# Performance work log

Measured on AMD Instinct MI355X. Metric: run time of the kernel, lower is better.

Reference implementation:

```python
import jax, jax.numpy as jnp
import numpy as np

L, B, E, H = 512, 4, 512, 8
D = E // H  # head_dim = 64


def setup_inputs() -> dict:
    key = jax.random.key(0)
    ks = jax.random.split(key, 7)
    query = jax.random.normal(ks[0], (L, B, E), dtype=jnp.float32)
    relation_k = jax.random.normal(ks[1], (B, L, L, D), dtype=jnp.float32)
    relation_v = jax.random.normal(ks[2], (B, L, L, D), dtype=jnp.float32)
    # xavier-uniform-ish scale for the fused QKV projection
    lim = float(np.sqrt(6.0 / (3 * E + E)))
    in_proj_weight = jax.random.uniform(ks[3], (3 * E, E), jnp.float32, -lim, lim)
    in_proj_bias = jnp.zeros((3 * E,), jnp.float32)
    lim_o = float(np.sqrt(1.0 / E))
    out_proj_weight = jax.random.uniform(ks[4], (E, E), jnp.float32, -lim_o, lim_o)
    out_proj_bias = jnp.zeros((E,), jnp.float32)
    return {
        "query": query,
        "relation_k": relation_k,
        "relation_v": relation_v,
        "in_proj_weight": in_proj_weight,
        "in_proj_bias": in_proj_bias,
        "out_proj_weight": out_proj_weight,
        "out_proj_bias": out_proj_bias,
    }


def reference(query, relation_k, relation_v, in_proj_weight, in_proj_bias,
              out_proj_weight, out_proj_bias):
    # query == key == value (qkv_same path), shape (L, B, E)
    scaling = float(D) ** -0.5
    qkv = query @ in_proj_weight.T + in_proj_bias          # (L, B, 3E)
    q, k, v = jnp.split(qkv, 3, axis=-1)                   # each (L, B, E)
    q = q * scaling

    def to_bhld(t):  # (L, B, E) -> (B, H, L, D)
        return t.reshape(L, B, H, D).transpose(1, 2, 0, 3)

    q, k, v = to_bhld(q), to_bhld(k), to_bhld(v)

    # content scores
    scores = jnp.einsum('bhid,bhjd->bhij', q, k)           # (B, H, L, L)

    # relation_k term: torch does a flat .view of (B*H, L, L, D) -> (B*H*L, D, L)
    # which is a row-major REINTERPRETATION (not a transpose). Replicate via reshape:
    rk = relation_k.reshape(B, L, D, L)                    # per-(b,i) block (L*D,) -> (D, L)
    scores = scores + jnp.einsum('bhid,bidj->bhij', q, rk)

    w = jax.nn.softmax(scores, axis=-1)
    w = jnp.where(jnp.isnan(w), jnp.zeros_like(w), w)      # NaN guard as in original

    out = jnp.einsum('bhij,bhjd->bhid', w, v)              # (B, H, L, D)
    # relation_v term: (B*H*L, 1, L) @ (B*H*L, L, D) -> per-query weighted relation values
    out = out + jnp.einsum('bhij,bijd->bhid', w, relation_v)

    out = out.transpose(2, 0, 1, 3).reshape(L, B, E)       # (B,H,L,D) -> (L,B,E)
    return out @ out_proj_weight.T + out_proj_bias
```

## Files before the change

### kernel.cpp

```cpp
#include <hip/hip_runtime.h>
#include <hip/hip_fp16.h>
#include <stdint.h>


typedef short short8 __attribute__((ext_vector_type(8)));
typedef float f32x4 __attribute__((ext_vector_type(4)));
typedef float f32x2 __attribute__((ext_vector_type(2)));
typedef unsigned short u16x4 __attribute__((ext_vector_type(4)));

static __device__ __forceinline__ uint16_t f2bf(float f) {
  uint32_t u = __float_as_uint(f);
  uint32_t r = (u + 0x7FFFu + ((u >> 16) & 1u)) >> 16;
  return (uint16_t)r;
}
static __device__ __forceinline__ float bf2f(uint16_t h) {
  return __uint_as_float(((uint32_t)h) << 16);
}
static __device__ __forceinline__ short8 ld8(const uint16_t* p) {
  return *(const short8*)p;
}
#define MFMA(a, b, c) __builtin_amdgcn_mfma_f32_16x16x32_bf16((a), (b), (c), 0, 0, 0)

__global__ __launch_bounds__(256) void k_conv_all(
    const float* __restrict__ in_w, const float* __restrict__ query,
    const float* __restrict__ out_w, uint16_t* __restrict__ w_hi,
    uint16_t* __restrict__ w_lo, uint16_t* __restrict__ a_hi,
    uint16_t* __restrict__ a_lo, uint16_t* __restrict__ wo_bf) {
  int e = (blockIdx.x * 256 + threadIdx.x) * 4;
  if (e < 786432) {
    f32x4 v = *(const f32x4*)(in_w + e);
    u16x4 hi, lo;
#pragma unroll
    for (int k = 0; k < 4; ++k) {
      hi[k] = f2bf(v[k]);
      lo[k] = f2bf(v[k] - bf2f(hi[k]));
    }
    *(u16x4*)(w_hi + e) = hi;
    *(u16x4*)(w_lo + e) = lo;
  } else if (e < 786432 + 1048576) {
    int o = e - 786432;
    f32x4 v = *(const f32x4*)(query + o);
    u16x4 hi, lo;
#pragma unroll
    for (int k = 0; k < 4; ++k) {
      hi[k] = f2bf(v[k]);
      lo[k] = f2bf(v[k] - bf2f(hi[k]));
    }
    *(u16x4*)(a_hi + o) = hi;
    *(u16x4*)(a_lo + o) = lo;
  } else {
    int o = e - 1835008;
    f32x4 v = *(const f32x4*)(out_w + o);
    u16x4 hi;
#pragma unroll
    for (int k = 0; k < 4; ++k) hi[k] = f2bf(v[k]);
    *(u16x4*)(wo_bf + o) = hi;
  }
}

__global__ __launch_bounds__(256) void k_inproj(
    const uint16_t* __restrict__ a_hi, const uint16_t* __restrict__ a_lo,
    const uint16_t* __restrict__ w_hi, const uint16_t* __restrict__ w_lo,
    const float* __restrict__ bias, float* __restrict__ q_s,
    uint16_t* __restrict__ q_bf, uint16_t* __restrict__ k_bf,
    uint16_t* __restrict__ v_bf) {
  const int wave = threadIdx.x >> 6, lane = threadIdx.x & 63;
  const int wr = wave >> 1, wc = wave & 1;
  const int rif = lane & 15, kg = lane >> 4;
  const int rbase = blockIdx.x * 64 + wr * 32;
  const int cbase = blockIdx.y * 64 + wc * 32;
  f32x4 acc[2][2] = {};
  for (int ks = 0; ks < 512; ks += 32) {
    int kofs = ks + kg * 8;
    short8 aH[2], aL[2], bH[2], bL[2];
#pragma unroll
    for (int m = 0; m < 2; ++m) {
      size_t idx = (size_t)(rbase + m * 16 + rif) * 512 + kofs;
      aH[m] = ld8(a_hi + idx);
      aL[m] = ld8(a_lo + idx);
    }
#pragma unroll
    for (int n = 0; n < 2; ++n) {
      size_t idx = (size_t)(cbase + n * 16 + rif) * 512 + kofs;
      bH[n] = ld8(w_hi + idx);
      bL[n] = ld8(w_lo + idx);
    }
#pragma unroll
    for (int m = 0; m < 2; ++m)
#pragma unroll
      for (int n = 0; n < 2; ++n) {
        acc[m][n] = MFMA(aH[m], bH[n], acc[m][n]);
        acc[m][n] = MFMA(aH[m], bL[n], acc[m][n]);
        acc[m][n] = MFMA(aL[m], bH[n], acc[m][n]);
      }
  }
#pragma unroll
  for (int m = 0; m < 2; ++m)
#pragma unroll
    for (int n = 0; n < 2; ++n)
#pragma unroll
      for (int r = 0; r < 4; ++r) {
        int row = rbase + m * 16 + kg * 4 + r;
        int col = cbase + n * 16 + rif;
        float val = acc[m][n][r] + bias[col];
        int l = row >> 2, b = row & 3;
        int sel = col >> 9, h = (col >> 6) & 7, d = col & 63;
        size_t oidx = ((size_t)(b * 8 + h) * 512 + l) * 64 + d;
        if (sel == 0) {
          val *= 0.125f;
          q_s[oidx] = val;
          q_bf[oidx] = f2bf(val);
        } else if (sel == 1) {
          k_bf[oidx] = f2bf(val);
        } else {
          v_bf[oidx] = f2bf(val);
        }
      }
}

__global__ __launch_bounds__(256) void k_scores(const uint16_t* __restrict__ q_bf,
                                                const uint16_t* __restrict__ k_bf,
                                                __half* __restrict__ scores) {
  const int bh = blockIdx.x;
  const uint16_t* qb = q_bf + (size_t)bh * 512 * 64;
  const uint16_t* kb = k_bf + (size_t)bh * 512 * 64;
  const int wave = threadIdx.x >> 6, lane = threadIdx.x & 63;
  const int wr = wave >> 1, wc = wave & 1;
  const int rif = lane & 15, kg = lane >> 4;
  const int ibase = blockIdx.y * 64 + wr * 32;
  const int jbase = blockIdx.z * 64 + wc * 32;
  f32x4 acc[2][2] = {};
#pragma unroll
  for (int ks = 0; ks < 64; ks += 32) {
    int kofs = ks + kg * 8;
    short8 A[2], Bb[2];
#pragma unroll
    for (int m = 0; m < 2; ++m) A[m] = ld8(qb + (size_t)(ibase + m * 16 + rif) * 64 + kofs);
#pragma unroll
    for (int n = 0; n < 2; ++n) Bb[n] = ld8(kb + (size_t)(jbase + n * 16 + rif) * 64 + kofs);
#pragma unroll
    for (int m = 0; m < 2; ++m)
#pragma unroll
      for (int n = 0; n < 2; ++n) acc[m][n] = MFMA(A[m], Bb[n], acc[m][n]);
  }
  __half* sc = scores + (size_t)bh * 512 * 512;
#pragma unroll
  for (int m = 0; m < 2; ++m)
#pragma unroll
    for (int n = 0; n < 2; ++n)
#pragma unroll
      for (int r = 0; r < 4; ++r)
        sc[(size_t)(ibase + m * 16 + kg * 4 + r) * 512 + (jbase + n * 16 + rif)] =
            __float2half(acc[m][n][r]);
}

__global__ __launch_bounds__(256, 8) void k_mega(
    const float* __restrict__ relation_k, const float* __restrict__ relation_v,
    const float* __restrict__ q_s, const __half* __restrict__ scores,
    uint16_t* __restrict__ wprob, uint16_t* __restrict__ rv_bf) {
  __shared__ float regA[4096];
  __shared__ float qv[512];
  const int b = blockIdx.x >> 9, i = blockIdx.x & 511;
  const int t = threadIdx.x;
  const int wave = t >> 6, lane = t & 63;
  for (int e = t; e < 512; e += 256) {
    int h = e >> 6, d = e & 63;
    qv[d * 8 + h] = q_s[(((size_t)b * 8 + h) * 512 + i) * 64 + d];
  }
  __syncthreads();
  {
    const float* rkp = relation_k + ((size_t)b * 512 + i) * 32768 + 2 * t;
    f32x2 acc[8] = {};
    for (int d0 = 0; d0 < 64; d0 += 8) {
      f32x2 kv[8];
#pragma unroll
      for (int u = 0; u < 8; ++u) kv[u] = *(const f32x2*)(rkp + (size_t)(d0 + u) * 512);
#pragma unroll
      for (int u = 0; u < 8; ++u) {
        f32x4 qA = *(const f32x4*)&qv[(d0 + u) * 8];
        f32x4 qB = *(const f32x4*)&qv[(d0 + u) * 8 + 4];
#pragma unroll
        for (int h = 0; h < 4; ++h) {
          acc[h].x += qA[h] * kv[u].x;
          acc[h].y += qA[h] * kv[u].y;
          acc[4 + h].x += qB[h] * kv[u].x;
          acc[4 + h].y += qB[h] * kv[u].y;
        }
      }
    }
#pragma unroll
    for (int h = 0; h < 8; ++h) *(f32x2*)&regA[h * 512 + 2 * t] = acc[h];
  }
  __syncthreads();
  float ex[2][8], rsum[2];
#pragma unroll
  for (int hh = 0; hh < 2; ++hh) {
    int h = wave * 2 + hh;
    const __half* srow = scores + (((size_t)b * 8 + h) * 512 + i) * 512;
    float s[8], m = -1e30f;
#pragma unroll
    for (int jj = 0; jj < 8; ++jj) {
      int j = jj * 64 + lane;
      s[jj] = __half2float(srow[j]) + regA[h * 512 + j];
      m = fmaxf(m, s[jj]);
    }
    for (int o = 32; o > 0; o >>= 1) m = fmaxf(m, __shfl_xor(m, o));
    float sum = 0.f;
#pragma unroll
    for (int jj = 0; jj < 8; ++jj) {
      ex[hh][jj] = __expf(s[jj] - m);
      sum += ex[hh][jj];
    }
    for (int o = 32; o > 0; o >>= 1) sum += __shfl_xor(sum, o);
    rsum[hh] = 1.f / sum;
  }
  __syncthreads();
  {
    float* pbf = regA;
#pragma unroll
    for (int jj = 0; jj < 8; ++jj) {
      int j = jj * 64 + lane;
      f32x2 p;
      p.x = ex[0][jj] * rsum[0];
      p.y = ex[1][jj] * rsum[1];
      *(f32x2*)&pbf[j * 8 + wave * 2] = p;
    }
#pragma unroll
    for (int hh = 0; hh < 2; ++hh) {
      int h = wave * 2 + hh;
      uint16_t* wrow = wprob + (((size_t)b * 8 + h) * 512 + i) * 512;
#pragma unroll
      for (int jj = 0; jj < 8; ++jj) wrow[jj * 64 + lane] = f2bf(ex[hh][jj] * rsum[hh]);
    }
  }
  __syncthreads();
  float racc[8] = {};
  {
    const float* pbf = regA;
    const float* rvb = relation_v + ((size_t)b * 512 + i) * 32768;
    const int jb = wave * 128;
    for (int jj = 0; jj < 128; jj += 8) {
      float r[8];
#pragma unroll
      for (int u = 0; u < 8; ++u) r[u] = rvb[(size_t)(jb + jj + u) * 64 + lane];
#pragma unroll
      for (int u = 0; u < 8; ++u) {
        f32x4 w0 = *(const f32x4*)&pbf[(jb + jj + u) * 8];
        f32x4 w1 = *(const f32x4*)&pbf[(jb + jj + u) * 8 + 4];
#pragma unroll
        for (int h = 0; h < 4; ++h) {
          racc[h] += w0[h] * r[u];
          racc[4 + h] += w1[h] * r[u];
        }
      }
    }
  }
  __syncthreads();
#pragma unroll
  for (int h = 0; h < 8; ++h) regA[(wave * 8 + h) * 64 + lane] = racc[h];
  __syncthreads();
  for (int e = t; e < 512; e += 256) {
    int h = e >> 6, d = e & 63;
    float s = regA[(0 * 8 + h) * 64 + d] + regA[(1 * 8 + h) * 64 + d] +
              regA[(2 * 8 + h) * 64 + d] + regA[(3 * 8 + h) * 64 + d];
    rv_bf[((size_t)i * 4 + b) * 512 + h * 64 + d] = f2bf(s);
  }
}

__global__ __launch_bounds__(256) void k_pv(const uint16_t* __restrict__ w_bf,
                                            const uint16_t* __restrict__ v_bf,
                                            uint16_t* __restrict__ pv_bf) {
  const int bh = blockIdx.x;
  const int b = bh >> 3, h = bh & 7;
  const uint16_t* wb = w_bf + (size_t)bh * 512 * 512;
  const uint16_t* vb = v_bf + (size_t)bh * 512 * 64;
  const int wave = threadIdx.x >> 6, lane = threadIdx.x & 63;
  const int wr = wave >> 1, wc = wave & 1;
  const int rif = lane & 15, kg = lane >> 4;
  const int ibase = blockIdx.y * 64 + wr * 32;
  const int dbase = wc * 32;
  f32x4 acc[2][2] = {};
  for (int ks = 0; ks < 512; ks += 32) {
    int kofs = ks + kg * 8;
    short8 A[2], Bb[2];
#pragma unroll
    for (int m = 0; m < 2; ++m) A[m] = ld8(wb + (size_t)(ibase + m * 16 + rif) * 512 + kofs);
#pragma unroll
    for (int n = 0; n < 2; ++n) {
      uint16_t tb[8];
#pragma unroll
      for (int e = 0; e < 8; ++e) tb[e] = vb[(size_t)(kofs + e) * 64 + dbase + n * 16 + rif];
      Bb[n] = *(const short8*)tb;
    }
#pragma unroll
    for (int m = 0; m < 2; ++m)
#pragma unroll
      for (int n = 0; n < 2; ++n) acc[m][n] = MFMA(A[m], Bb[n], acc[m][n]);
  }
#pragma unroll
  for (int m = 0; m < 2; ++m)
#pragma unroll
    for (int n = 0; n < 2; ++n)
#pragma unroll
      for (int r = 0; r < 4; ++r) {
        int i = ibase + m * 16 + kg * 4 + r;
        int d = dbase + n * 16 + rif;
        pv_bf[((size_t)i * 4 + b) * 512 + h * 64 + d] = f2bf(acc[m][n][r]);
      }
}

__global__ __launch_bounds__(256) void k_outproj(const uint16_t* __restrict__ rv_a,
                                                 const uint16_t* __restrict__ pv_a,
                                                 const uint16_t* __restrict__ wo_bf,
                                                 const float* __restrict__ bias,
                                                 float* __restrict__ out) {
  const int wave = threadIdx.x >> 6, lane = threadIdx.x & 63;
  const int wr = wave >> 1, wc = wave & 1;
  const int rif = lane & 15, kg = lane >> 4;
  const int rbase = blockIdx.x * 64 + wr * 32;
  const int cbase = blockIdx.y * 64 + wc * 32;
  f32x4 acc[2][2] = {};
  for (int ks = 0; ks < 512; ks += 32) {
    int kofs = ks + kg * 8;
    short8 A[2], Bb[2];
#pragma unroll
    for (int m = 0; m < 2; ++m) {
      size_t idx = (size_t)(rbase + m * 16 + rif) * 512 + kofs;
      short8 p = ld8(pv_a + idx);
      short8 rr = ld8(rv_a + idx);
      uint16_t tb[8];
#pragma unroll
      for (int e = 0; e < 8; ++e)
        tb[e] = f2bf(bf2f((uint16_t)p[e]) + bf2f((uint16_t)rr[e]));
      A[m] = *(const short8*)tb;
    }
#pragma unroll
    for (int n = 0; n < 2; ++n) Bb[n] = ld8(wo_bf + (size_t)(cbase + n * 16 + rif) * 512 + kofs);
#pragma unroll
    for (int m = 0; m < 2; ++m)
#pragma unroll
      for (int n = 0; n < 2; ++n) acc[m][n] = MFMA(A[m], Bb[n], acc[m][n]);
  }
#pragma unroll
  for (int m = 0; m < 2; ++m)
#pragma unroll
    for (int n = 0; n < 2; ++n)
#pragma unroll
      for (int r = 0; r < 4; ++r) {
        int row = rbase + m * 16 + kg * 4 + r;
        int col = cbase + n * 16 + rif;
        out[(size_t)row * 512 + col] = acc[m][n][r] + bias[col];
      }
}

extern "C" void kernel_launch(void* const* d_in, const int* in_sizes, int n_in,
                              void* d_out, int out_size, void* d_ws, size_t ws_size,
                              hipStream_t stream) {
  const float* query = (const float*)d_in[0];
  const float* relation_k = (const float*)d_in[1];
  const float* relation_v = (const float*)d_in[2];
  const float* in_w = (const float*)d_in[3];
  const float* in_b = (const float*)d_in[4];
  const float* out_w = (const float*)d_in[5];
  const float* out_b = (const float*)d_in[6];
  float* out = (float*)d_out;
  char* ws = (char*)d_ws;

  uint16_t* a_hi  = (uint16_t*)(ws + 0);
  uint16_t* a_lo  = (uint16_t*)(ws + 2097152);
  uint16_t* w_hi  = (uint16_t*)(ws + 4194304);
  uint16_t* w_lo  = (uint16_t*)(ws + 5767168);
  uint16_t* wo_bf = (uint16_t*)(ws + 7340032);
  float*    q_s   = (float*)   (ws + 7864320);
  uint16_t* q_bf  = (uint16_t*)(ws + 12058624);
  uint16_t* k_bf  = (uint16_t*)(ws + 14155776);
  uint16_t* v_bf  = (uint16_t*)(ws + 16252928);
  uint16_t* rv_bf = (uint16_t*)(ws + 18350080);
  uint16_t* pv_bf = (uint16_t*)(ws + 20447232);
  uint16_t* wprob = (uint16_t*)(ws + 22544384);
  __half*   sc_h  = (__half*)  (ws + 39321600);

  k_conv_all<<<dim3(2048), 256, 0, stream>>>(in_w, query, out_w, w_hi, w_lo, a_hi, a_lo, wo_bf);
  k_inproj<<<dim3(32, 24), 256, 0, stream>>>(a_hi, a_lo, w_hi, w_lo, in_b, q_s, q_bf, k_bf, v_bf);
  k_scores<<<dim3(32, 8, 8), 256, 0, stream>>>(q_bf, k_bf, sc_h);
  k_mega<<<dim3(2048), 256, 0, stream>>>(relation_k, relation_v, q_s, sc_h, wprob, rv_bf);
  k_pv<<<dim3(32, 8), 256, 0, stream>>>(wprob, v_bf, pv_bf);
  k_outproj<<<dim3(32, 8), 256, 0, stream>>>(rv_bf, pv_bf, wo_bf, out_b, out);
}
```

Measured before the change: 205.5 us.

## Vectorize relation_k/relation_v streaming with 16-byte loads and split-D reduction in mega kernel

Rewrites the fused relation kernel so each thread loads float4 chunks of relation_k and relation_v instead of float2 or scalar loads. The relation_k pass is split across waves by head-dim halves and combined through padded shared memory. The relation_v pass now splits lanes over j and d with a shuffle reduction. The launch-bounds occupancy hint is dropped and the wprob global store is moved ahead of a barrier. The aim is better bandwidth on the dominant HBM stream of relation tensors, at the cost of higher register pressure and extra shared-memory reduction steps.

```diff
diff --git a/kernel.cpp b/kernel.cpp
--- a/kernel.cpp
+++ b/kernel.cpp
@@ -5,7 +5,6 @@
 
 typedef short short8 __attribute__((ext_vector_type(8)));
 typedef float f32x4 __attribute__((ext_vector_type(4)));
-typedef float f32x2 __attribute__((ext_vector_type(2)));
 typedef unsigned short u16x4 __attribute__((ext_vector_type(4)));
 
 static __device__ __forceinline__ uint16_t f2bf(float f) {
@@ -154,42 +153,56 @@
             __float2half(acc[m][n][r]);
 }
 
-__global__ __launch_bounds__(256, 8) void k_mega(
+__global__ __launch_bounds__(256) void k_mega2(
     const float* __restrict__ relation_k, const float* __restrict__ relation_v,
     const float* __restrict__ q_s, const __half* __restrict__ scores,
     uint16_t* __restrict__ wprob, uint16_t* __restrict__ rv_bf) {
-  __shared__ float regA[4096];
-  __shared__ float qv[512];
+  __shared__ float qh[512];
+  __shared__ float shr[4608];
   const int b = blockIdx.x >> 9, i = blockIdx.x & 511;
   const int t = threadIdx.x;
   const int wave = t >> 6, lane = t & 63;
   for (int e = t; e < 512; e += 256) {
     int h = e >> 6, d = e & 63;
-    qv[d * 8 + h] = q_s[(((size_t)b * 8 + h) * 512 + i) * 64 + d];
-  }
-  __syncthreads();
+    qh[d * 8 + h] = q_s[(((size_t)b * 8 + h) * 512 + i) * 64 + d];
+  }
+  __syncthreads();
+  const int H = wave & 1, Dh = wave >> 1;
+  const int j0 = H * 256 + lane * 4;
+  f32x4 acc[8];
+#pragma unroll
+  for (int h = 0; h < 8; ++h) acc[h] = f32x4{0.f, 0.f, 0.f, 0.f};
   {
-    const float* rkp = relation_k + ((size_t)b * 512 + i) * 32768 + 2 * t;
-    f32x2 acc[8] = {};
-    for (int d0 = 0; d0 < 64; d0 += 8) {
-      f32x2 kv[8];
-#pragma unroll
-      for (int u = 0; u < 8; ++u) kv[u] = *(const f32x2*)(rkp + (size_t)(d0 + u) * 512);
-#pragma unroll
-      for (int u = 0; u < 8; ++u) {
-        f32x4 qA = *(const f32x4*)&qv[(d0 + u) * 8];
-        f32x4 qB = *(const f32x4*)&qv[(d0 + u) * 8 + 4];
-#pragma unroll
-        for (int h = 0; h < 4; ++h) {
-          acc[h].x += qA[h] * kv[u].x;
-          acc[h].y += qA[h] * kv[u].y;
-          acc[4 + h].x += qB[h] * kv[u].x;
-          acc[4 + h].y += qB[h] * kv[u].y;
-        }
-      }
-    }
-#pragma unroll
-    for (int h = 0; h < 8; ++h) *(f32x2*)&regA[h * 512 + 2 * t] = acc[h];
+    const float* rkp =
+        relation_k + ((size_t)b * 512 + i) * 32768 + (size_t)Dh * 32 * 512 + j0;
+    const float* qp = qh + Dh * 32 * 8;
+#pragma unroll 2
+    for (int dd = 0; dd < 32; ++dd) {
+      f32x4 kv = *(const f32x4*)(rkp + (size_t)dd * 512);
+      f32x4 qA = *(const f32x4*)(qp + dd * 8);
+      f32x4 qB = *(const f32x4*)(qp + dd * 8 + 4);
+#pragma unroll
+      for (int h = 0; h < 4; ++h) {
+        acc[h] += qA[h] * kv;
+        acc[4 + h] += qB[h] * kv;
+      }
+    }
+  }
+  if (Dh == 1) {
+#pragma unroll
+    for (int h = 0; h < 8; ++h)
+      *(f32x4*)&shr[(H * 64 + lane) * 33 + h * 4] = acc[h];
+  }
+  __syncthreads();
+  if (Dh == 0) {
+#pragma unroll
+    for (int h = 0; h < 8; ++h)
+      acc[h] += *(const f32x4*)&shr[(H * 64 + lane) * 33 + h * 4];
+  }
+  __syncthreads();
+  if (Dh == 0) {
+#pragma unroll
+    for (int h = 0; h < 8; ++h) *(f32x4*)&shr[h * 512 + j0] = acc[h];
   }
   __syncthreads();
   float ex[2][8], rsum[2];
@@ -201,7 +214,7 @@
 #pragma unroll
     for (int jj = 0; jj < 8; ++jj) {
       int j = jj * 64 + lane;
-      s[jj] = __half2float(srow[j]) + regA[h * 512 + j];
+      s[jj] = __half2float(srow[j]) + shr[h * 512 + j];
       m = fmaxf(m, s[jj]);
     }
     for (int o = 32; o > 0; o >>= 1) m = fmaxf(m, __shfl_xor(m, o));
@@ -214,55 +227,61 @@
     for (int o = 32; o > 0; o >>= 1) sum += __shfl_xor(sum, o);
     rsum[hh] = 1.f / sum;
   }
-  __syncthreads();
-  {
-    float* pbf = regA;
+#pragma unroll
+  for (int hh = 0; hh < 2; ++hh) {
+    int h = wave * 2 + hh;
+    uint16_t* wrow = wprob + (((size_t)b * 8 + h) * 512 + i) * 512;
+#pragma unroll
+    for (int jj = 0; jj < 8; ++jj) wrow[jj * 64 + lane] = f2bf(ex[hh][jj] * rsum[hh]);
+  }
+  __syncthreads();
+#pragma unroll
+  for (int hh = 0; hh < 2; ++hh) {
+    int h = wave * 2 + hh;
 #pragma unroll
     for (int jj = 0; jj < 8; ++jj) {
       int j = jj * 64 + lane;
-      f32x2 p;
-      p.x = ex[0][jj] * rsum[0];
-      p.y = ex[1][jj] * rsum[1];
-      *(f32x2*)&pbf[j * 8 + wave * 2] = p;
-    }
-#pragma unroll
-    for (int hh = 0; hh < 2; ++hh) {
-      int h = wave * 2 + hh;
-      uint16_t* wrow = wprob + (((size_t)b * 8 + h) * 512 + i) * 512;
-#pragma unroll
-      for (int jj = 0; jj < 8; ++jj) wrow[jj * 64 + lane] = f2bf(ex[hh][jj] * rsum[hh]);
-    }
-  }
-  __syncthreads();
-  float racc[8] = {};
+      shr[j * 9 + h] = ex[hh][jj] * rsum[hh];
+    }
+  }
+  __syncthreads();
+  f32x4 racc[8];
+#pragma unroll
+  for (int h = 0; h < 8; ++h) racc[h] = f32x4{0.f, 0.f, 0.f, 0.f};
   {
-    const float* pbf = regA;
+    const int jsub = lane >> 4, d4 = (lane & 15) * 4;
     const float* rvb = relation_v + ((size_t)b * 512 + i) * 32768;
-    const int jb = wave * 128;
-    for (int jj = 0; jj < 128; jj += 8) {
-      float r[8];
-#pragma unroll
-      for (int u = 0; u < 8; ++u) r[u] = rvb[(size_t)(jb + jj + u) * 64 + lane];
-#pragma unroll
-      for (int u = 0; u < 8; ++u) {
-        f32x4 w0 = *(const f32x4*)&pbf[(jb + jj + u) * 8];
-        f32x4 w1 = *(const f32x4*)&pbf[(jb + jj + u) * 8 + 4];
-#pragma unroll
-        for (int h = 0; h < 4; ++h) {
-          racc[h] += w0[h] * r[u];
-          racc[4 + h] += w1[h] * r[u];
-        }
-      }
-    }
-  }
-  __syncthreads();
-#pragma unroll
-  for (int h = 0; h < 8; ++h) regA[(wave * 8 + h) * 64 + lane] = racc[h];
+#pragma unroll 2
+    for (int s = 0; s < 32; ++s) {
+      int j = s * 16 + wave * 4 + jsub;
+      f32x4 rvv = *(const f32x4*)(rvb + (size_t)j * 64 + d4);
+      f32x4 w0 = *(const f32x4*)&shr[j * 9];
+      f32x4 w1 = *(const f32x4*)&shr[j * 9 + 4];
+#pragma unroll
+      for (int h = 0; h < 4; ++h) {
+        racc[h] += w0[h] * rvv;
+        racc[4 + h] += w1[h] * rvv;
+      }
+    }
+  }
+#pragma unroll
+  for (int h = 0; h < 8; ++h)
+#pragma unroll
+    for (int c = 0; c < 4; ++c) {
+      racc[h][c] += __shfl_xor(racc[h][c], 16);
+      racc[h][c] += __shfl_xor(racc[h][c], 32);
+    }
+  __syncthreads();
+  if (lane < 16) {
+#pragma unroll
+    for (int h = 0; h < 8; ++h)
+      *(f32x4*)&shr[(wave * 8 + h) * 64 + (lane & 15) * 4] = racc[h];
+  }
   __syncthreads();
   for (int e = t; e < 512; e += 256) {
     int h = e >> 6, d = e & 63;
-    float s = regA[(0 * 8 + h) * 64 + d] + regA[(1 * 8 + h) * 64 + d] +
-              regA[(2 * 8 + h) * 64 + d] + regA[(3 * 8 + h) * 64 + d];
+    float s = shr[(0 * 8 + h) * 64 + d] + shr[(1 * 8 + h) * 64 + d] +
+              shr[(2 * 8 + h) * 64 + d] + shr[(3 * 8 + h) * 64 + d];
     rv_bf[((size_t)i * 4 + b) * 512 + h * 64 + d] = f2bf(s);
   }
 }
@@ -383,7 +402,7 @@
   k_conv_all<<<dim3(2048), 256, 0, stream>>>(in_w, query, out_w, w_hi, w_lo, a_hi, a_lo, wo_bf);
   k_inproj<<<dim3(32, 24), 256, 0, stream>>>(a_hi, a_lo, w_hi, w_lo, in_b, q_s, q_bf, k_bf, v_bf);
   k_scores<<<dim3(32, 8, 8), 256, 0, stream>>>(q_bf, k_bf, sc_h);
-  k_mega<<<dim3(2048), 256, 0, stream>>>(relation_k, relation_v, q_s, sc_h, wprob, rv_bf);
+  k_mega2<<<dim3(2048), 256, 0, stream>>>(relation_k, relation_v, q_s, sc_h, wprob, rv_bf);
   k_pv<<<dim3(32, 8), 256, 0, stream>>>(wprob, v_bf, pv_bf);
   k_outproj<<<dim3(32, 8), 256, 0, stream>>>(rv_bf, pv_bf, wo_bf, out_b, out);
 }
```

After: 211.8 us. +3.1%, slower.
